# Performance work log

Measured on AMD Instinct MI355X. Metric: run time of the kernel, lower is better.

Reference implementation:

```python
import jax, jax.numpy as jnp
import numpy as np

C = 64
R = 16

def setup_inputs() -> dict:
    key = jax.random.key(0)
    k0, k1, k2, k3, k4 = jax.random.split(key, 5)
    x = jax.random.normal(k0, (4, C, 32, 128, 128), dtype=jnp.float32)
    # 1x1x1 conv weights expressed as dense matrices
    w1 = jax.random.normal(k1, (C // R, C), dtype=jnp.float32) * (1.0 / np.sqrt(C))
    b1 = jax.random.normal(k2, (C // R,), dtype=jnp.float32) * 0.01
    w2 = jax.random.normal(k3, (C, C // R), dtype=jnp.float32) * (1.0 / np.sqrt(C // R))
    b2 = jax.random.normal(k4, (C,), dtype=jnp.float32) * 0.01
    return {"x": x, "w1": w1, "b1": b1, "w2": w2, "b2": b2}

def reference(x, w1, b1, w2, b2):
    # x: [B, C, D, H, W]
    mean = jnp.mean(x, axis=(2, 3, 4))                       # [B, C]
    var = jnp.mean((x - mean[:, :, None, None, None]) ** 2,
                   axis=(2, 3, 4))                           # [B, C] (biased)
    std = jnp.sqrt(var)
    y = std + mean                                           # contrast + avg_pool, [B, C]
    h = jax.nn.relu(jnp.einsum('rc,bc->br', w1, y) + b1)     # [B, C//R]
    g = jax.nn.sigmoid(jnp.einsum('cr,br->bc', w2, h) + b2)  # [B, C]
    return x * g[:, :, None, None, None]
```

## Files before the change

kernel.cpp:

```cpp
#include <hip/hip_runtime.h>
#include <math.h>


#define CCH 64
#define BATCH 4
#define NCH (BATCH * CCH)
#define SPATIAL (32 * 128 * 128)
#define NVEC (SPATIAL / 4)

#define BPC1 16
#define BPC3 64

__global__ __launch_bounds__(256) void cca_stats(const float* __restrict__ x,
                                                 double* __restrict__ sums) {
    const int bc  = blockIdx.x / BPC1;
    const int blk = blockIdx.x % BPC1;
    const float4* xc = (const float4*)(x + (size_t)bc * SPATIAL);
    const int per_block = NVEC / BPC1;
    const int base = blk * per_block;

    float s1 = 0.f, s2 = 0.f;
    for (int i = threadIdx.x; i < per_block; i += 256) {
        float4 v = xc[base + i];
        s1 += (v.x + v.y) + (v.z + v.w);
        s2 += (v.x * v.x + v.y * v.y) + (v.z * v.z + v.w * v.w);
    }

    double d1 = (double)s1, d2 = (double)s2;
    #pragma unroll
    for (int off = 32; off > 0; off >>= 1) {
        d1 += __shfl_down(d1, off, 64);
        d2 += __shfl_down(d2, off, 64);
    }
    __shared__ double sh1[4], sh2[4];
    const int wave = threadIdx.x >> 6;
    const int lane = threadIdx.x & 63;
    if (lane == 0) { sh1[wave] = d1; sh2[wave] = d2; }
    __syncthreads();
    if (threadIdx.x == 0) {
        double t1 = (sh1[0] + sh1[1]) + (sh1[2] + sh1[3]);
        double t2 = (sh2[0] + sh2[1]) + (sh2[2] + sh2[3]);
        atomicAdd(&sums[bc * 2 + 0], t1);
        atomicAdd(&sums[bc * 2 + 1], t2);
    }
}

__global__ __launch_bounds__(256) void cca_mlp(const double* __restrict__ sums,
                                               const float* __restrict__ w1,
                                               const float* __restrict__ b1,
                                               const float* __restrict__ w2,
                                               const float* __restrict__ b2,
                                               float* __restrict__ g) {
    __shared__ float y[NCH];
    __shared__ float h[BATCH][4];
    const int t = threadIdx.x;

    if (t < NCH) {
        double s1 = sums[t * 2 + 0];
        double s2 = sums[t * 2 + 1];
        double mean = s1 / (double)SPATIAL;
        double var  = s2 / (double)SPATIAL - mean * mean;
        if (var < 0.0) var = 0.0;
        y[t] = (float)(sqrt(var) + mean);
    }
    __syncthreads();

    if (t < BATCH * 4) {
        const int b = t >> 2, r = t & 3;
        float acc = b1[r];
        #pragma unroll
        for (int c = 0; c < CCH; ++c) acc += w1[r * CCH + c] * y[b * CCH + c];
        h[b][r] = acc > 0.f ? acc : 0.f;
    }
    __syncthreads();

    if (t < NCH) {
        const int b = t / CCH, c = t % CCH;
        float acc = b2[c];
        #pragma unroll
        for (int r = 0; r < 4; ++r) acc += w2[c * 4 + r] * h[b][r];
        g[t] = 1.f / (1.f + __expf(-acc));
    }
}

__global__ __launch_bounds__(256) void cca_scale(const float* __restrict__ x,
                                                 const float* __restrict__ g,
                                                 float* __restrict__ out) {
    const int bc  = blockIdx.x / BPC3;
    const int blk = blockIdx.x % BPC3;
    const float gv = g[bc];
    const int per_block = NVEC / BPC3;
    const size_t base = (size_t)bc * NVEC + (size_t)blk * per_block;
    const float4* xv = (const float4*)x;
    float4* ov = (float4*)out;
    #pragma unroll 4
    for (int i = threadIdx.x; i < per_block; i += 256) {
        float4 v = xv[base + i];
        v.x *= gv; v.y *= gv; v.z *= gv; v.w *= gv;
        ov[base + i] = v;
    }
}

extern "C" void kernel_launch(void* const* d_in, const int* in_sizes, int n_in,
                              void* d_out, int out_size, void* d_ws, size_t ws_size,
                              hipStream_t stream) {
    const float* x  = (const float*)d_in[0];
    const float* w1 = (const float*)d_in[1];
    const float* b1 = (const float*)d_in[2];
    const float* w2 = (const float*)d_in[3];
    const float* b2 = (const float*)d_in[4];
    float* out = (float*)d_out;

    double* sums = (double*)d_ws;
    float* g = (float*)((char*)d_ws + NCH * 2 * sizeof(double));

    hipMemsetAsync(d_ws, 0, NCH * 2 * sizeof(double), stream);

    cca_stats<<<NCH * BPC1, 256, 0, stream>>>(x, sums);
    cca_mlp<<<1, 256, 0, stream>>>(sums, w1, b1, w2, b2, g);
    cca_scale<<<NCH * BPC3, 256, 0, stream>>>(x, g, out);
}
```

Baseline: 941.7 us.

## Replace atomics with per-block partials, unroll loads, reverse scale order, nontemporal stores

The stats kernel now writes per-block partial sums to a workspace array instead of double atomics, which removes the memset launch. The MLP kernel reduces those partials. Stats loads are fully unrolled with split accumulators for more memory-level parallelism. The scale kernel walks blocks in reverse so it touches the most recently read data first, aiming for L2/MALL reuse, and it uses nontemporal stores to avoid polluting the cache with output.

```diff
diff --git a/kernel.cpp b/kernel.cpp
--- a/kernel.cpp
+++ b/kernel.cpp
@@ -11,22 +11,34 @@
 #define BPC1 16
 #define BPC3 64
 
+typedef float vfloat4 __attribute__((ext_vector_type(4)));
+
 __global__ __launch_bounds__(256) void cca_stats(const float* __restrict__ x,
-                                                 double* __restrict__ sums) {
+                                                 double2* __restrict__ part) {
     const int bc  = blockIdx.x / BPC1;
     const int blk = blockIdx.x % BPC1;
-    const float4* xc = (const float4*)(x + (size_t)bc * SPATIAL);
-    const int per_block = NVEC / BPC1;
-    const int base = blk * per_block;
+    const float4* p = (const float4*)(x + (size_t)bc * SPATIAL)
+                    + (size_t)blk * (NVEC / BPC1) + threadIdx.x;
 
-    float s1 = 0.f, s2 = 0.f;
-    for (int i = threadIdx.x; i < per_block; i += 256) {
-        float4 v = xc[base + i];
-        s1 += (v.x + v.y) + (v.z + v.w);
-        s2 += (v.x * v.x + v.y * v.y) + (v.z * v.z + v.w * v.w);
+    float s1a = 0.f, s2a = 0.f, s1b = 0.f, s2b = 0.f;
+    #pragma unroll
+    for (int k = 0; k < 32; k += 4) {
+        float4 v0 = p[(k + 0) * 256];
+        float4 v1 = p[(k + 1) * 256];
+        float4 v2 = p[(k + 2) * 256];
+        float4 v3 = p[(k + 3) * 256];
+        s1a += (v0.x + v0.y) + (v0.z + v0.w);
+        s2a += (v0.x * v0.x + v0.y * v0.y) + (v0.z * v0.z + v0.w * v0.w);
+        s1b += (v1.x + v1.y) + (v1.z + v1.w);
+        s2b += (v1.x * v1.x + v1.y * v1.y) + (v1.z * v1.z + v1.w * v1.w);
+        s1a += (v2.x + v2.y) + (v2.z + v2.w);
+        s2a += (v2.x * v2.x + v2.y * v2.y) + (v2.z * v2.z + v2.w * v2.w);
+        s1b += (v3.x + v3.y) + (v3.z + v3.w);
+        s2b += (v3.x * v3.x + v3.y * v3.y) + (v3.z * v3.z + v3.w * v3.w);
     }
 
-    double d1 = (double)s1, d2 = (double)s2;
+    double d1 = (double)s1a + (double)s1b;
+    double d2 = (double)s2a + (double)s2b;
     #pragma unroll
     for (int off = 32; off > 0; off >>= 1) {
         d1 += __shfl_down(d1, off, 64);
@@ -34,18 +46,16 @@
     }
     __shared__ double sh1[4], sh2[4];
     const int wave = threadIdx.x >> 6;
-    const int lane = threadIdx.x & 63;
-    if (lane == 0) { sh1[wave] = d1; sh2[wave] = d2; }
+    if ((threadIdx.x & 63) == 0) { sh1[wave] = d1; sh2[wave] = d2; }
     __syncthreads();
     if (threadIdx.x == 0) {
         double t1 = (sh1[0] + sh1[1]) + (sh1[2] + sh1[3]);
         double t2 = (sh2[0] + sh2[1]) + (sh2[2] + sh2[3]);
-        atomicAdd(&sums[bc * 2 + 0], t1);
-        atomicAdd(&sums[bc * 2 + 1], t2);
+        part[bc * BPC1 + blk] = make_double2(t1, t2);
     }
 }
 
-__global__ __launch_bounds__(256) void cca_mlp(const double* __restrict__ sums,
+__global__ __launch_bounds__(256) void cca_mlp(const double2* __restrict__ part,
                                                const float* __restrict__ w1,
                                                const float* __restrict__ b1,
                                                const float* __restrict__ w2,
@@ -55,14 +65,16 @@
     __shared__ float h[BATCH][4];
     const int t = threadIdx.x;
 
-    if (t < NCH) {
-        double s1 = sums[t * 2 + 0];
-        double s2 = sums[t * 2 + 1];
-        double mean = s1 / (double)SPATIAL;
-        double var  = s2 / (double)SPATIAL - mean * mean;
-        if (var < 0.0) var = 0.0;
-        y[t] = (float)(sqrt(var) + mean);
+    double s1 = 0.0, s2 = 0.0;
+    #pragma unroll
+    for (int k = 0; k < BPC1; ++k) {
+        double2 pv = part[t * BPC1 + k];
+        s1 += pv.x; s2 += pv.y;
     }
+    double mean = s1 / (double)SPATIAL;
+    double var  = s2 / (double)SPATIAL - mean * mean;
+    if (var < 0.0) var = 0.0;
+    y[t] = (float)(sqrt(var) + mean);
     __syncthreads();
 
     if (t < BATCH * 4) {
@@ -74,7 +86,7 @@
     }
     __syncthreads();
 
-    if (t < NCH) {
+    {
         const int b = t / CCH, c = t % CCH;
         float acc = b2[c];
         #pragma unroll
@@ -86,18 +98,19 @@
 __global__ __launch_bounds__(256) void cca_scale(const float* __restrict__ x,
                                                  const float* __restrict__ g,
                                                  float* __restrict__ out) {
-    const int bc  = blockIdx.x / BPC3;
-    const int blk = blockIdx.x % BPC3;
+    const int gid = (int)gridDim.x - 1 - (int)blockIdx.x;
+    const int bc  = gid / BPC3;
+    const int blk = gid % BPC3;
     const float gv = g[bc];
-    const int per_block = NVEC / BPC3;
-    const size_t base = (size_t)bc * NVEC + (size_t)blk * per_block;
-    const float4* xv = (const float4*)x;
-    float4* ov = (float4*)out;
-    #pragma unroll 4
-    for (int i = threadIdx.x; i < per_block; i += 256) {
-        float4 v = xv[base + i];
-        v.x *= gv; v.y *= gv; v.z *= gv; v.w *= gv;
-        ov[base + i] = v;
+    const size_t base = (size_t)bc * NVEC + (size_t)blk * (NVEC / BPC3)
+                      + threadIdx.x;
+    const vfloat4* xv = (const vfloat4*)x + base;
+    vfloat4* ov = (vfloat4*)out + base;
+    #pragma unroll
+    for (int k = 0; k < 8; ++k) {
+        vfloat4 v = xv[k * 256];
+        v *= gv;
+        __builtin_nontemporal_store(v, ov + k * 256);
     }
 }
 
@@ -111,12 +124,10 @@
     const float* b2 = (const float*)d_in[4];
     float* out = (float*)d_out;
 
-    double* sums = (double*)d_ws;
-    float* g = (float*)((char*)d_ws + NCH * 2 * sizeof(double));
+    double2* part = (double2*)d_ws;
+    float* g = (float*)((char*)d_ws + (size_t)NCH * BPC1 * sizeof(double2));
 
-    hipMemsetAsync(d_ws, 0, NCH * 2 * sizeof(double), stream);
-
-    cca_stats<<<NCH * BPC1, 256, 0, stream>>>(x, sums);
-    cca_mlp<<<1, 256, 0, stream>>>(sums, w1, b1, w2, b2, g);
+    cca_stats<<<NCH * BPC1, 256, 0, stream>>>(x, part);
+    cca_mlp<<<1, 256, 0, stream>>>(part, w1, b1, w2, b2, g);
     cca_scale<<<NCH * BPC3, 256, 0, stream>>>(x, g, out);
 }
```

Result: no change. 937.5 us (-0.4%).
